# Performance work log

Measured on AMD Instinct MI355X. Metric: run time of the kernel, lower is better.

Reference implementation:

```python
import jax, jax.numpy as jnp
import numpy as np

NSAMPLE = 64
RADIUS = 0.3
HMIN = -0.2
HMAX_LIST = (0.1, 0.2, 0.3, 0.4)
NUM_ANGLE = 12
NUM_DEPTH = 4
EPS = 1e-5


def setup_inputs() -> dict:
    key = jax.random.key(0)
    ks = jax.random.split(key, 32)
    rn = lambda i, s: jax.random.normal(ks[i], s, dtype=jnp.float32)
    ru = lambda i, s: jax.random.uniform(ks[i], s, dtype=jnp.float32)
    return {
        'seed_xyz': rn(0, (2, 1024, 3)),
        'pointcloud': rn(1, (2, 8192, 3)),
        'vp_rot': rn(2, (2, 1024, 3, 3)),
        'cw1': rn(3, (64, 3)), 'cbn1': ru(4, (4, 64)),
        'cw2': rn(5, (128, 64)), 'cbn2': ru(6, (4, 128)),
        'cw3': rn(7, (256, 128)), 'cbn3': ru(8, (4, 256)),
        'ow1': rn(9, (128, 256)), 'ob1': rn(10, (128,)), 'obn1': ru(11, (4, 128)),
        'ow2': rn(12, (128, 128)), 'ob2': rn(13, (128,)), 'obn2': ru(14, (4, 128)),
        'ow3': rn(15, (36, 128)), 'ob3': rn(16, (36,)),
        'tw1': rn(17, (128, 256)), 'tb1': rn(18, (128,)), 'tbn1': ru(19, (4, 128)),
        'tw2': rn(20, (128, 128)), 'tb2': rn(21, (128,)), 'tbn2': ru(22, (4, 128)),
        'tw3': rn(23, (12, 128)), 'tb3': rn(24, (12,)),
    }


def _bn_relu(y, bn):
    g, b, m, v = bn[0], bn[1], bn[2], bn[3]
    return jax.nn.relu(g * (y - m) * jax.lax.rsqrt(v + EPS) + b)


def _bn(y, bn):
    g, b, m, v = bn[0], bn[1], bn[2], bn[3]
    return g * (y - m) * jax.lax.rsqrt(v + EPS) + b


def _forward(seed_xyz, pointcloud, vp_rot, cw1, cbn1, cw2, cbn2, cw3, cbn3,
             ow1, ob1, obn1, ow2, ob2, obn2, ow3, ob3,
             tw1, tb1, tbn1, tw2, tb2, tbn2, tw3, tb3):
    B, ns, _ = seed_xyz.shape
    N = pointcloud.shape[1]
    # relative coords of every scene point w.r.t. every seed, rotated into the
    # grasp-view frame (cylinder axis = x after rotation): (B, ns, N, 3)
    rel = pointcloud[:, None, :, :] - seed_xyz[:, :, None, :]
    rot_rel = jnp.einsum('bsnc,bscd->bsnd', rel, vp_rot)
    ax = rot_rel[..., 0]
    r2 = rot_rel[..., 1] ** 2 + rot_rel[..., 2] ** 2
    pref = jnp.arange(N, dtype=jnp.float32) / N  # earlier index preferred (CUDA scan order)
    groups = []
    for hmax in HMAX_LIST:
        mask = (ax > HMIN) & (ax < hmax) & (r2 < RADIUS * RADIUS)
        score = mask.astype(jnp.float32) * 2.0 - pref
        _, idx = jax.lax.top_k(score, NSAMPLE)  # (B, ns, NSAMPLE), first valid idxs in order
        valid = jnp.take_along_axis(mask, idx, axis=-1)
        idx = jnp.where(valid, idx, idx[..., :1])  # fill slots with first found index
        g = jnp.take_along_axis(rot_rel, idx[..., None], axis=2)  # (B, ns, NSAMPLE, 3)
        groups.append(g)
    feat = jnp.stack(groups, axis=2)  # (B, ns, num_depth, NSAMPLE, 3)
    feat = feat.reshape(B, ns * NUM_DEPTH, NSAMPLE, 3)
    # SharedMLP [3,64,128,256], conv2d 1x1 (no bias) + BN + ReLU
    h = _bn_relu(feat @ cw1.T, cbn1)
    h = _bn_relu(h @ cw2.T, cbn2)
    h = _bn_relu(h @ cw3.T, cbn3)
    vp = jnp.max(h, axis=2)  # max-pool over nsample -> (B, ns*num_depth, 256)

    def head(w1, b1, bn1, w2, b2, bn2, w3, b3):
        x = _bn_relu(vp @ w1.T + b1, bn1)
        x = _bn_relu(x @ w2.T + b2, bn2)
        return x @ w3.T + b3

    op = head(ow1, ob1, obn1, ow2, ob2, obn2, ow3, ob3)     # (B, ns*D, 3*num_angle)
    tol = head(tw1, tb1, tbn1, tw2, tb2, tbn2, tw3, tb3)    # (B, ns*D, num_angle)
    out = jnp.concatenate([op, tol], axis=-1)               # score|angle_cls|width|tolerance
    out = out.reshape(B, ns, NUM_DEPTH, 4 * NUM_ANGLE).transpose(0, 3, 1, 2)
    return out  # (B, 4*num_angle, num_seed, num_depth)


def reference(seed_xyz, pointcloud, vp_rot, cw1, cbn1, cw2, cbn2, cw3, cbn3,
              ow1, ob1, obn1, ow2, ob2, obn2, ow3, ob3,
              tw1, tb1, tbn1, tw2, tb2, tbn2, tw3, tb3):
    return _forward(seed_xyz, pointcloud, vp_rot, cw1, cbn1, cw2, cbn2, cw3, cbn3,
                    ow1, ob1, obn1, ow2, ob2, obn2, ow3, ob3,
                    tw1, tb1, tbn1, tw2, tb2, tbn2, tw3, tb3)
```

## Files before the change

kernel.cpp:

```cpp
#include <hip/hip_runtime.h>
#include <hip/hip_bf16.h>

#define NB    2
#define NS    1024
#define NPTS  8192
#define NGROUP (NB*NS*4)

enum : int {
  OFF_BW2  = 256,
  OFF_W1Q  = 4352,
  OFF_B2   = 8448,
  OFF_BW3  = 8576,
  OFF_B3   = 41344,
  OFF_HB1  = 41600,
  OFF_HB1B = 74368,
  OFF_HB2  = 74624,
  OFF_HB2B = 107392,
  OFF_HB3  = 107648,
  OFF_HB3B = 115840,
  OFF_FEAT = 146688,
  OFF_VP   = 1719552,
  OFF_PCX  = 1719552,
  OFF_PCY  = 1735936,
  OFF_PCZ  = 1752320,
  OFF_SEED = 1768704,
  OFF_ROT  = 1774848,
  OFF_FLAG = 3824896,
  PREP_TOTAL = 189632 + 6144 + 18432 + 49152,
};

struct Ptrs { const void* p[25]; };

typedef __attribute__((ext_vector_type(8))) short bf16x8;
typedef __attribute__((ext_vector_type(4))) float f32x4;
typedef __attribute__((ext_vector_type(4))) unsigned u32x4;

template<typename T> struct LD;
template<> struct LD<float> {
  static __device__ __forceinline__ float get(const void* p, int i){ return ((const float*)p)[i]; }
};
template<> struct LD<__hip_bfloat16> {
  static __device__ __forceinline__ float get(const void* p, int i){ return __bfloat162float(((const __hip_bfloat16*)p)[i]); }
};

template<typename T>
__device__ __forceinline__ float bnscale(const void* bn, int C, int c){
  float g = LD<T>::get(bn, c);
  float v = LD<T>::get(bn, 3*C + c);
  return g / sqrtf(v + 1e-5f);
}

__device__ __forceinline__ unsigned short f2bf(float v){
  __hip_bfloat16 hb = __float2bfloat16(v);
  return *reinterpret_cast<unsigned short*>(&hb);
}

#if __has_builtin(__builtin_amdgcn_cvt_pk_bf16_f32)
typedef __attribute__((ext_vector_type(2))) __bf16 bf16x2_t;
__device__ __forceinline__ unsigned pk2bf(float a, float b){
  bf16x2_t r = __builtin_amdgcn_cvt_pk_bf16_f32(a, b);
  return *reinterpret_cast<unsigned*>(&r);
}
#else
__device__ __forceinline__ unsigned pk2bf(float a, float b){
  return (unsigned)f2bf(a) | ((unsigned)f2bf(b) << 16);
}
#endif

template<typename T>
__device__ void prep_body(const Ptrs& in, float* __restrict__ ws, int i){
  if (i < 256) { int c = i>>2, d = i&3; float s = bnscale<T>(in.p[4],64,c);
    float v = (d<3) ? LD<T>::get(in.p[3], c*3+d)*s
                    : LD<T>::get(in.p[4],64+c) - LD<T>::get(in.p[4],2*64+c)*s;
    ws[OFF_W1Q+i] = v; return; }
  i -= 256;
  if (i < 8192) {
    int j = i&7, f = i>>3, lane = f&63, kn = f>>6, kt = kn&1, nt = kn>>1;
    int n = nt*16 + (lane&15), k = kt*32 + ((lane>>4)<<3) + j;
    float s = bnscale<T>(in.p[6],128,n);
    ((unsigned short*)(ws + OFF_BW2))[i] = f2bf(LD<T>::get(in.p[5], n*64+k)*s); return; }
  i -= 8192;
  if (i < 32768) {
    int j = i&7, f = i>>3, lane = f&63, kn = f>>6, kt = kn&3, nt = kn>>2;
    int n = nt*16 + (lane&15), k = kt*32 + ((lane>>4)<<3) + j;
    float s = bnscale<T>(in.p[8],256,n);
    ((unsigned short*)(ws + OFF_BW3))[i] = f2bf(LD<T>::get(in.p[7], n*128+k)*s); return; }
  i -= 32768;
  if (i < 128) { float s = bnscale<T>(in.p[6],128,i);
    ws[OFF_B2+i] = LD<T>::get(in.p[6],128+i) - LD<T>::get(in.p[6],2*128+i)*s; return; }
  i -= 128;
  if (i < 256) { float s = bnscale<T>(in.p[8],256,i);
    ws[OFF_B3+i] = LD<T>::get(in.p[8],256+i) - LD<T>::get(in.p[8],2*256+i)*s; return; }
  i -= 256;
  if (i < 65536) {
    int j = i&7, f = i>>3, lane = f&63, kn = f>>6, kt = kn&7, nt = kn>>3;
    int n = nt*16 + (lane&15), k = kt*32 + ((lane>>4)<<3) + j;
    float v;
    if (n < 128) v = LD<T>::get(in.p[9],  n*256+k)       * bnscale<T>(in.p[11],128,n);
    else         v = LD<T>::get(in.p[17], (n-128)*256+k) * bnscale<T>(in.p[19],128,n-128);
    ((unsigned short*)(ws + OFF_HB1))[i] = f2bf(v); return; }
  i -= 65536;
  if (i < 256) { int n = i; float v;
    if (n < 128) { float s = bnscale<T>(in.p[11],128,n);
      v = (LD<T>::get(in.p[10],n) - LD<T>::get(in.p[11],2*128+n))*s + LD<T>::get(in.p[11],128+n); }
    else { int m = n-128; float s = bnscale<T>(in.p[19],128,m);
      v = (LD<T>::get(in.p[18],m) - LD<T>::get(in.p[19],2*128+m))*s + LD<T>::get(in.p[19],128+m); }
    ws[OFF_HB1B+n] = v; return; }
  i -= 256;
  if (i < 65536) {
    int j = i&7, f = i>>3, lane = f&63, kn = f>>6, kt = kn&7, nt = kn>>3;
    int n = nt*16 + (lane&15), k = kt*32 + ((lane>>4)<<3) + j;
    float v = 0.f;
    if (n < 128) { if (k < 128)  v = LD<T>::get(in.p[12], n*128+k)            * bnscale<T>(in.p[14],128,n); }
    else         { if (k >= 128) v = LD<T>::get(in.p[20], (n-128)*128+(k-128)) * bnscale<T>(in.p[22],128,n-128); }
    ((unsigned short*)(ws + OFF_HB2))[i] = f2bf(v); return; }
  i -= 65536;
  if (i < 256) { int n = i; float v;
    if (n < 128) { float s = bnscale<T>(in.p[14],128,n);
      v = (LD<T>::get(in.p[13],n) - LD<T>::get(in.p[14],2*128+n))*s + LD<T>::get(in.p[14],128+n); }
    else { int m = n-128; float s = bnscale<T>(in.p[22],128,m);
      v = (LD<T>::get(in.p[21],m) - LD<T>::get(in.p[22],2*128+m))*s + LD<T>::get(in.p[22],128+m); }
    ws[OFF_HB2B+n] = v; return; }
  i -= 256;
  if (i < 16384) {
    int j = i&7, f = i>>3, lane = f&63, kn = f>>6, kt = kn&7, nt = kn>>3;
    int n = nt*16 + (lane&15), k = kt*32 + ((lane>>4)<<3) + j;
    float v = 0.f;
    if (n < 36)      { if (k < 128)  v = LD<T>::get(in.p[15], n*128+k); }
    else if (n < 48) { if (k >= 128) v = LD<T>::get(in.p[23], (n-36)*128+(k-128)); }
    ((unsigned short*)(ws + OFF_HB3))[i] = f2bf(v); return; }
  i -= 16384;
  if (i < 64) { int n = i; float v = 0.f;
    if (n < 36) v = LD<T>::get(in.p[16], n);
    else if (n < 48) v = LD<T>::get(in.p[24], n-36);
    ws[OFF_HB3B+n] = v; return; }
  i -= 64;
  if (i < 6144)  { ws[OFF_SEED+i] = LD<T>::get(in.p[0], i); return; }
  i -= 6144;
  if (i < 18432) { ws[OFF_ROT+i] = LD<T>::get(in.p[2], i); return; }
  i -= 18432;
  {
    int arr = i >> 14, idx = i & 16383;
    ws[OFF_PCX + arr*16384 + idx] = LD<T>::get(in.p[1], idx*3 + arr); }
}

__global__ __launch_bounds__(256) void prep_kernel(Ptrs in, float* __restrict__ ws){
  __shared__ int sf;
  const int t = threadIdx.x;
  if (t == 0) sf = 0;
  __syncthreads();
  int loc = 0;
  const uint4* w3r = (const uint4*)in.p[7];
#pragma unroll
  for (int k = 0; k < 8; ++k) {
    uint4 u = w3r[t + k*256];
    loc |= ((u.x & 0x7F80u) == 0x7F80u) | (((u.x>>16) & 0x7F80u) == 0x7F80u);
    loc |= ((u.y & 0x7F80u) == 0x7F80u) | (((u.y>>16) & 0x7F80u) == 0x7F80u);
    loc |= ((u.z & 0x7F80u) == 0x7F80u) | (((u.z>>16) & 0x7F80u) == 0x7F80u);
    loc |= ((u.w & 0x7F80u) == 0x7F80u) | (((u.w>>16) & 0x7F80u) == 0x7F80u);
  }
  if (loc) atomicOr(&sf, 1);
  __syncthreads();
  const int isf32 = sf;
  const int i = blockIdx.x*256 + t;
  if (i == 0) ((int*)(ws + OFF_FLAG))[0] = isf32;
  if (i >= PREP_TOTAL) return;
  if (isf32) prep_body<float>(in, ws, i);
  else       prep_body<__hip_bfloat16>(in, ws, i);
}

__global__ __launch_bounds__(256) void group_kernel(float* __restrict__ ws){
#pragma clang fp contract(off)
  __shared__ float scratch[2][2][4][192];
  __shared__ int   cl[2][2][4];
  __shared__ float p0s[2][3];
  const int t = threadIdx.x;
  const int wave = t >> 6, lane = t & 63;
  const int s = wave >> 1, half = wave & 1;
  const int seedIdx = blockIdx.x*2 + s;
  const int b = seedIdx >> 10;
  const float sx = ws[OFF_SEED + seedIdx*3+0];
  const float sy = ws[OFF_SEED + seedIdx*3+1];
  const float sz = ws[OFF_SEED + seedIdx*3+2];
  const float r00=ws[OFF_ROT+seedIdx*9+0], r01=ws[OFF_ROT+seedIdx*9+1], r02=ws[OFF_ROT+seedIdx*9+2];
  const float r10=ws[OFF_ROT+seedIdx*9+3], r11=ws[OFF_ROT+seedIdx*9+4], r12=ws[OFF_ROT+seedIdx*9+5];
  const float r20=ws[OFF_ROT+seedIdx*9+6], r21=ws[OFF_ROT+seedIdx*9+7], r22=ws[OFF_ROT+seedIdx*9+8];
  const float* px = ws + OFF_PCX + b*8192;
  const float* py = ws + OFF_PCY + b*8192;
  const float* pz = ws + OFF_PCZ + b*8192;
  if (half == 0 && lane == 0) {
    float e0 = px[0] - sx, e1 = py[0] - sy, e2 = pz[0] - sz;
    p0s[s][0] = e0*r00 + e1*r10 + e2*r20;
    p0s[s][1] = e0*r01 + e1*r11 + e2*r21;
    p0s[s][2] = e0*r02 + e1*r12 + e2*r22;
  }
  float* s0 = scratch[s][half][0];
  float* s1 = scratch[s][half][1];
  float* s2 = scratch[s][half][2];
  float* s3 = scratch[s][half][3];
  int c0n=0, c1n=0, c2n=0, c3n=0;
  const int basept = half*4096;
  const unsigned long long pm = (1ull << lane) - 1ull;

  auto scan = [&](float x, float y, float z){
    float e0 = x - sx, e1 = y - sy, e2 = z - sz;
    float rx = e0*r00 + e1*r10 + e2*r20;
    float ry = e0*r01 + e1*r11 + e2*r21;
    float rz = e0*r02 + e1*r12 + e2*r22;
    float r2 = ry*ry + rz*rz;
    const bool mb = (rx > -0.2f) && (r2 < 0.09f);
    { bool m = mb && (rx < 0.1f); unsigned long long bal = __ballot(m);
      if (bal) { int slot = c0n + __popcll(bal & pm);
        if (m && slot < 64) { s0[slot*3]=rx; s0[slot*3+1]=ry; s0[slot*3+2]=rz; }
        c0n += __popcll(bal); } }
    { bool m = mb && (rx < 0.2f); unsigned long long bal = __ballot(m);
      if (bal) { int slot = c1n + __popcll(bal & pm);
        if (m && slot < 64) { s1[slot*3]=rx; s1[slot*3+1]=ry; s1[slot*3+2]=rz; }
        c1n += __popcll(bal); } }
    { bool m = mb && (rx < 0.3f); unsigned long long bal = __ballot(m);
      if (bal) { int slot = c2n + __popcll(bal & pm);
        if (m && slot < 64) { s2[slot*3]=rx; s2[slot*3+1]=ry; s2[slot*3+2]=rz; }
        c2n += __popcll(bal); } }
    { bool m = mb && (rx < 0.4f); unsigned long long bal = __ballot(m);
      if (bal) { int slot = c3n + __popcll(bal & pm);
        if (m && slot < 64) { s3[slot*3]=rx; s3[slot*3+1]=ry; s3[slot*3+2]=rz; }
        c3n += __popcll(bal); } }
  };

  for (int c = 0; c < 64; c += 2) {
    const int i0 = basept + c*64 + lane;
    float xA = px[i0],    yA = py[i0],    zA = pz[i0];
    float xB = px[i0+64], yB = py[i0+64], zB = pz[i0+64];
    scan(xA, yA, zA);
    scan(xB, yB, zB);
  }
  if (lane == 0) { cl[s][half][0]=c0n; cl[s][half][1]=c1n; cl[s][half][2]=c2n; cl[s][half][3]=c3n; }
  __syncthreads();
  for (int idx = t; idx < 512; idx += 256) {
    const int ss = idx >> 8, bin = (idx >> 6) & 3, slot = idx & 63;
    int ca = cl[ss][0][bin]; if (ca > 64) ca = 64;
    int cb = cl[ss][1][bin];
    const float* A = scratch[ss][0][bin];
    const float* B = scratch[ss][1][bin];
    float fx, fy, fz;
    if (slot < ca)              { fx=A[slot*3]; fy=A[slot*3+1]; fz=A[slot*3+2]; }
    else if (slot - ca < cb)    { int q = slot-ca; fx=B[q*3]; fy=B[q*3+1]; fz=B[q*3+2]; }
    else if (ca > 0)            { fx=A[0]; fy=A[1]; fz=A[2]; }
    else if (cb > 0)            { fx=B[0]; fy=B[1]; fz=B[2]; }
    else                        { fx=p0s[ss][0]; fy=p0s[ss][1]; fz=p0s[ss][2]; }
    const int g = (blockIdx.x*2 + ss)*4 + bin;
    float* fo = ws + OFF_FEAT + g*192;
    fo[slot*3+0]=fx; fo[slot*3+1]=fy; fo[slot*3+2]=fz;
  }
}

__global__ __launch_bounds__(256) void mlp_kernel(float* __restrict__ ws){
  __shared__ unsigned short h2s[2][64*136];
  __shared__ float w1q[4][256];
  const int t = threadIdx.x;
  const int wave = t >> 6, lane = t & 63;
  const int quad = lane >> 4, l15 = lane & 15;
  const int grp = wave >> 1, nhalf = wave & 1;
  const int g = blockIdx.x*2 + grp;
  for (int i = t; i < 1024; i += 256) w1q[i>>8][i&255] = ws[OFF_W1Q + (i&255)];
  const float* feat = ws + OFF_FEAT + g*192;
  __syncthreads();
  float fx[4], fy[4], fz[4];
#pragma unroll
  for (int Nt = 0; Nt < 4; ++Nt) {
    const int sm = Nt*16 + l15;
    fx[Nt] = feat[sm*3+0]; fy[Nt] = feat[sm*3+1]; fz[Nt] = feat[sm*3+2];
  }
  bf16x8 b1[4][2];
  const float* wq = w1q[quad];
#pragma unroll
  for (int kt = 0; kt < 2; ++kt) {
    f32x4 w[8];
#pragma unroll
    for (int j = 0; j < 8; ++j) w[j] = *(const f32x4*)(wq + (kt*32 + quad*8 + j)*4);
#pragma unroll
    for (int Nt = 0; Nt < 4; ++Nt) {
      const float x0 = fx[Nt], x1 = fy[Nt], x2 = fz[Nt];
      u32x4 p;
#pragma unroll
      for (int jp = 0; jp < 4; ++jp) {
        const f32x4 wa = w[2*jp], wb = w[2*jp+1];
        const float v0 = fmaxf(wa[3] + x0*wa[0] + x1*wa[1] + x2*wa[2], 0.f);
        const float v1 = fmaxf(wb[3] + x0*wb[0] + x1*wb[1] + x2*wb[2], 0.f);
        p[jp] = pk2bf(v0, v1);
      }
      b1[Nt][kt] = __builtin_bit_cast(bf16x8, p);
    }
  }
  unsigned short* h2 = h2s[grp];
  const bf16x8* BW2 = (const bf16x8*)(ws + OFF_BW2);
#pragma unroll
  for (int mt4 = 0; mt4 < 4; ++mt4) {
    const int Mt = nhalf*4 + mt4;
    const f32x4 bias4 = *(const f32x4*)(ws + OFF_B2 + Mt*16 + quad*4);
    f32x4 acc[4];
#pragma unroll
    for (int Nt = 0; Nt < 4; ++Nt) acc[Nt] = bias4;
#pragma unroll
    for (int kt = 0; kt < 2; ++kt) {
      const bf16x8 aw = BW2[(Mt*2+kt)*64 + lane];
#pragma unroll
      for (int Nt = 0; Nt < 4; ++Nt)
        acc[Nt] = __builtin_amdgcn_mfma_f32_16x16x32_bf16(aw, b1[Nt][kt], acc[Nt], 0, 0, 0);
    }
#pragma unroll
    for (int Nt = 0; Nt < 4; ++Nt) {
      const unsigned lo = pk2bf(fmaxf(acc[Nt][0],0.f), fmaxf(acc[Nt][1],0.f));
      const unsigned hi = pk2bf(fmaxf(acc[Nt][2],0.f), fmaxf(acc[Nt][3],0.f));
      uint2* dst = (uint2*)&h2[(Nt*16 + l15)*136 + Mt*16 + quad*4];
      *dst = make_uint2(lo, hi);
    }
  }
  __syncthreads();
  bf16x8 a2[4][4];
#pragma unroll
  for (int mt = 0; mt < 4; ++mt)
#pragma unroll
    for (int kt = 0; kt < 4; ++kt)
      a2[mt][kt] = *(const bf16x8*)&h2[(mt*16 + l15)*136 + kt*32 + quad*8];
  const bf16x8* BW3 = (const bf16x8*)(ws + OFF_BW3);
  float vpv[8];
#pragma unroll
  for (int nt8 = 0; nt8 < 8; ++nt8) {
    const int nt = nhalf*8 + nt8;
    const int n = nt*16 + l15;
    const float bias = ws[OFF_B3 + n];
    f32x4 acc[4];
#pragma unroll
    for (int mt = 0; mt < 4; ++mt) acc[mt] = (f32x4){bias, bias, bias, bias};
#pragma unroll
    for (int kt = 0; kt < 4; ++kt) {
      const bf16x8 b = BW3[(nt*4+kt)*64 + lane];
#pragma unroll
      for (int mt = 0; mt < 4; ++mt)
        acc[mt] = __builtin_amdgcn_mfma_f32_16x16x32_bf16(a2[mt][kt], b, acc[mt], 0, 0, 0);
    }
    float mx = 0.f;
#pragma unroll
    for (int mt = 0; mt < 4; ++mt) {
      mx = fmaxf(mx, fmaxf(fmaxf(acc[mt][0], acc[mt][1]), fmaxf(acc[mt][2], acc[mt][3])));
    }
    mx = fmaxf(mx, 0.f);
    mx = fmaxf(mx, __shfl_xor(mx, 16, 64));
    mx = fmaxf(mx, __shfl_xor(mx, 32, 64));
    vpv[nt8] = mx;
  }
  if (quad == 0) {
    float* vp = ws + OFF_VP + g*256 + nhalf*128;
#pragma unroll
    for (int nt8 = 0; nt8 < 8; ++nt8) vp[nt8*16 + l15] = vpv[nt8];
  }
}

#define YSTRIDE 264
__global__ __launch_bounds__(256) void heads_kernel(float* __restrict__ ws, void* __restrict__ outv){
  const int isf32 = ((const volatile int*)(ws + OFF_FLAG))[0];
  __shared__ unsigned short y[16*YSTRIDE];
  const int t = threadIdx.x;
  const int wave = t >> 6, lane = t & 63;
  const int quad = lane >> 4, l15 = lane & 15;
  const int r0 = blockIdx.x * 16;
  bf16x8 a[8];
  const float* vp = ws + OFF_VP + (r0 + l15)*256;
#pragma unroll
  for (int kt = 0; kt < 8; ++kt) {
    const float4* v4 = (const float4*)(vp + kt*32 + quad*8);
    float4 u0 = v4[0], u1 = v4[1];
    a[kt][0]=(short)f2bf(u0.x); a[kt][1]=(short)f2bf(u0.y); a[kt][2]=(short)f2bf(u0.z); a[kt][3]=(short)f2bf(u0.w);
    a[kt][4]=(short)f2bf(u1.x); a[kt][5]=(short)f2bf(u1.y); a[kt][6]=(short)f2bf(u1.z); a[kt][7]=(short)f2bf(u1.w);
  }
  const bf16x8* HB1 = (const bf16x8*)(ws + OFF_HB1);
#pragma unroll
  for (int nt4 = 0; nt4 < 4; ++nt4) {
    const int nt = wave*4 + nt4;
    const int n = nt*16 + l15;
    const float bias = ws[OFF_HB1B + n];
    f32x4 acc = (f32x4){bias, bias, bias, bias};
#pragma unroll
    for (int kt = 0; kt < 8; ++kt)
      acc = __builtin_amdgcn_mfma_f32_16x16x32_bf16(a[kt], HB1[(nt*8+kt)*64 + lane], acc, 0, 0, 0);
#pragma unroll
    for (int jj = 0; jj < 4; ++jj)
      y[(quad*4+jj)*YSTRIDE + n] = f2bf(fmaxf(acc[jj], 0.f));
  }
  __syncthreads();
#pragma unroll
  for (int kt = 0; kt < 8; ++kt)
    a[kt] = *(const bf16x8*)&y[l15*YSTRIDE + kt*32 + quad*8];
  __syncthreads();
  const bf16x8* HB2 = (const bf16x8*)(ws + OFF_HB2);
#pragma unroll
  for (int nt4 = 0; nt4 < 4; ++nt4) {
    const int nt = wave*4 + nt4;
    const int n = nt*16 + l15;
    const float bias = ws[OFF_HB2B + n];
    f32x4 acc = (f32x4){bias, bias, bias, bias};
#pragma unroll
    for (int kt = 0; kt < 8; ++kt)
      acc = __builtin_amdgcn_mfma_f32_16x16x32_bf16(a[kt], HB2[(nt*8+kt)*64 + lane], acc, 0, 0, 0);
#pragma unroll
    for (int jj = 0; jj < 4; ++jj)
      y[(quad*4+jj)*YSTRIDE + n] = f2bf(fmaxf(acc[jj], 0.f));
  }
  __syncthreads();
#pragma unroll
  for (int kt = 0; kt < 8; ++kt)
    a[kt] = *(const bf16x8*)&y[l15*YSTRIDE + kt*32 + quad*8];
  const bf16x8* HB3 = (const bf16x8*)(ws + OFF_HB3);
  {
    const int n = wave*16 + l15;
    const float bias = ws[OFF_HB3B + n];
    f32x4 acc = (f32x4){bias, bias, bias, bias};
#pragma unroll
    for (int kt = 0; kt < 8; ++kt)
      acc = __builtin_amdgcn_mfma_f32_16x16x32_bf16(a[kt], HB3[(wave*8+kt)*64 + lane], acc, 0, 0, 0);
    if (n < 48) {
#pragma unroll
      for (int jj = 0; jj < 4; ++jj) {
        const int gr = r0 + quad*4 + jj;
        const int b = gr >> 12, rem = gr & 4095, s = rem >> 2, d = rem & 3;
        const int o = ((b*48 + n)*1024 + s)*4 + d;
        if (isf32) ((float*)outv)[o] = acc[jj];
        else       ((__hip_bfloat16*)outv)[o] = __float2bfloat16(acc[jj]);
      }
    }
  }
}

extern "C" void kernel_launch(void* const* d_in, const int* in_sizes, int n_in,
                              void* d_out, int out_size, void* d_ws, size_t ws_size,
                              hipStream_t stream) {
  float* ws = (float*)d_ws;
  Ptrs P;
  for (int i = 0; i < 25; ++i) P.p[i] = d_in[i];
  prep_kernel<<<(PREP_TOTAL+255)/256, 256, 0, stream>>>(P, ws);
  group_kernel<<<NB*NS/2, 256, 0, stream>>>(ws);
  mlp_kernel<<<NGROUP/2, 256, 0, stream>>>(ws);
  heads_kernel<<<NGROUP/16, 256, 0, stream>>>(ws, d_out);
}
```

Measured before the change: 204.9 us.

## Bucket groups by valid-sample count and run MLP only on needed row tiles

The grouping kernel now counts valid neighbours per group and atomically appends each group to one of four buckets, keyed by how many 16-row tiles it needs. The MLP kernel is templated on the tile count and launched over all buckets. Each block reads its group ids from the bucket list and only runs the MFMA work for the occupied tiles. This is exact because padded samples repeat an earlier point and cannot change the max-pool. It removes wasted matrix work on sparse groups, at the cost of atomics, an indirect group lookup and many early-exit blocks in an oversized grid.

```diff
diff --git a/kernel.cpp b/kernel.cpp
--- a/kernel.cpp
+++ b/kernel.cpp
@@ -20,12 +20,11 @@
   OFF_HB3B = 115840,
   OFF_FEAT = 146688,
   OFF_VP   = 1719552,
-  OFF_PCX  = 1719552,
-  OFF_PCY  = 1735936,
-  OFF_PCZ  = 1752320,
-  OFF_SEED = 1768704,
-  OFF_ROT  = 1774848,
+  OFF_PCX  = 1719552, OFF_PCY = 1735936, OFF_PCZ = 1752320,
+  OFF_SEED = 1768704, OFF_ROT = 1774848,
   OFF_FLAG = 3824896,
+  OFF_BCNT = 3824900,
+  OFF_BL   = 3824912,
   PREP_TOTAL = 189632 + 6144 + 18432 + 49152,
 };
 
@@ -139,8 +138,7 @@
   i -= 6144;
   if (i < 18432) { ws[OFF_ROT+i] = LD<T>::get(in.p[2], i); return; }
   i -= 18432;
-  {
-    int arr = i >> 14, idx = i & 16383;
+  { int arr = i >> 14, idx = i & 16383;
     ws[OFF_PCX + arr*16384 + idx] = LD<T>::get(in.p[1], idx*3 + arr); }
 }
 
@@ -163,7 +161,10 @@
   __syncthreads();
   const int isf32 = sf;
   const int i = blockIdx.x*256 + t;
-  if (i == 0) ((int*)(ws + OFF_FLAG))[0] = isf32;
+  if (blockIdx.x == 0) {
+    if (t == 0) ((int*)(ws + OFF_FLAG))[0] = isf32;
+    if (t < 4)  ((int*)(ws + OFF_BCNT))[t] = 0;
+  }
   if (i >= PREP_TOTAL) return;
   if (isf32) prep_body<float>(in, ws, i);
   else       prep_body<__hip_bfloat16>(in, ws, i);
@@ -252,34 +253,37 @@
     float* fo = ws + OFF_FEAT + g*192;
     fo[slot*3+0]=fx; fo[slot*3+1]=fy; fo[slot*3+2]=fz;
   }
-}
-
-__global__ __launch_bounds__(256) void mlp_kernel(float* __restrict__ ws){
-  __shared__ unsigned short h2s[2][64*136];
-  __shared__ float w1q[4][256];
-  const int t = threadIdx.x;
-  const int wave = t >> 6, lane = t & 63;
-  const int quad = lane >> 4, l15 = lane & 15;
-  const int grp = wave >> 1, nhalf = wave & 1;
-  const int g = blockIdx.x*2 + grp;
-  for (int i = t; i < 1024; i += 256) w1q[i>>8][i&255] = ws[OFF_W1Q + (i&255)];
+  if (t < 8) {
+    const int ss = t >> 2, bin = t & 3;
+    int tot = cl[ss][0][bin] + cl[ss][1][bin];
+    if (tot > 64) tot = 64;
+    if (tot < 1)  tot = 1;
+    const int mt = (tot + 15) >> 4;
+    const int g = (blockIdx.x*2 + ss)*4 + bin;
+    int w = atomicAdd(&((int*)(ws + OFF_BCNT))[mt-1], 1);
+    if (w < 8192) ((int*)(ws + OFF_BL))[(mt-1)*8192 + w] = g;
+  }
+}
+
+template<int MTS>
+__device__ __forceinline__ void mlp_body(float* __restrict__ ws, unsigned short* __restrict__ h2,
+                                         const float* __restrict__ wq,
+                                         int lane, int quad, int l15, int nhalf, int g){
   const float* feat = ws + OFF_FEAT + g*192;
-  __syncthreads();
-  float fx[4], fy[4], fz[4];
-#pragma unroll
-  for (int Nt = 0; Nt < 4; ++Nt) {
+  float fx[MTS], fy[MTS], fz[MTS];
+#pragma unroll
+  for (int Nt = 0; Nt < MTS; ++Nt) {
     const int sm = Nt*16 + l15;
     fx[Nt] = feat[sm*3+0]; fy[Nt] = feat[sm*3+1]; fz[Nt] = feat[sm*3+2];
   }
-  bf16x8 b1[4][2];
-  const float* wq = w1q[quad];
+  bf16x8 b1[MTS][2];
 #pragma unroll
   for (int kt = 0; kt < 2; ++kt) {
     f32x4 w[8];
 #pragma unroll
     for (int j = 0; j < 8; ++j) w[j] = *(const f32x4*)(wq + (kt*32 + quad*8 + j)*4);
 #pragma unroll
-    for (int Nt = 0; Nt < 4; ++Nt) {
+    for (int Nt = 0; Nt < MTS; ++Nt) {
       const float x0 = fx[Nt], x1 = fy[Nt], x2 = fz[Nt];
       u32x4 p;
 #pragma unroll
@@ -292,24 +296,23 @@
       b1[Nt][kt] = __builtin_bit_cast(bf16x8, p);
     }
   }
-  unsigned short* h2 = h2s[grp];
   const bf16x8* BW2 = (const bf16x8*)(ws + OFF_BW2);
 #pragma unroll
   for (int mt4 = 0; mt4 < 4; ++mt4) {
     const int Mt = nhalf*4 + mt4;
     const f32x4 bias4 = *(const f32x4*)(ws + OFF_B2 + Mt*16 + quad*4);
-    f32x4 acc[4];
-#pragma unroll
-    for (int Nt = 0; Nt < 4; ++Nt) acc[Nt] = bias4;
+    f32x4 acc[MTS];
+#pragma unroll
+    for (int Nt = 0; Nt < MTS; ++Nt) acc[Nt] = bias4;
 #pragma unroll
     for (int kt = 0; kt < 2; ++kt) {
       const bf16x8 aw = BW2[(Mt*2+kt)*64 + lane];
 #pragma unroll
-      for (int Nt = 0; Nt < 4; ++Nt)
+      for (int Nt = 0; Nt < MTS; ++Nt)
         acc[Nt] = __builtin_amdgcn_mfma_f32_16x16x32_bf16(aw, b1[Nt][kt], acc[Nt], 0, 0, 0);
     }
 #pragma unroll
-    for (int Nt = 0; Nt < 4; ++Nt) {
+    for (int Nt = 0; Nt < MTS; ++Nt) {
       const unsigned lo = pk2bf(fmaxf(acc[Nt][0],0.f), fmaxf(acc[Nt][1],0.f));
       const unsigned hi = pk2bf(fmaxf(acc[Nt][2],0.f), fmaxf(acc[Nt][3],0.f));
       uint2* dst = (uint2*)&h2[(Nt*16 + l15)*136 + Mt*16 + quad*4];
@@ -317,9 +320,9 @@
     }
   }
   __syncthreads();
-  bf16x8 a2[4][4];
-#pragma unroll
-  for (int mt = 0; mt < 4; ++mt)
+  bf16x8 a2[MTS][4];
+#pragma unroll
+  for (int mt = 0; mt < MTS; ++mt)
 #pragma unroll
     for (int kt = 0; kt < 4; ++kt)
       a2[mt][kt] = *(const bf16x8*)&h2[(mt*16 + l15)*136 + kt*32 + quad*8];
@@ -330,22 +333,20 @@
     const int nt = nhalf*8 + nt8;
     const int n = nt*16 + l15;
     const float bias = ws[OFF_B3 + n];
-    f32x4 acc[4];
-#pragma unroll
-    for (int mt = 0; mt < 4; ++mt) acc[mt] = (f32x4){bias, bias, bias, bias};
+    f32x4 acc[MTS];
+#pragma unroll
+    for (int mt = 0; mt < MTS; ++mt) acc[mt] = (f32x4){bias, bias, bias, bias};
 #pragma unroll
     for (int kt = 0; kt < 4; ++kt) {
       const bf16x8 b = BW3[(nt*4+kt)*64 + lane];
 #pragma unroll
-      for (int mt = 0; mt < 4; ++mt)
+      for (int mt = 0; mt < MTS; ++mt)
         acc[mt] = __builtin_amdgcn_mfma_f32_16x16x32_bf16(a2[mt][kt], b, acc[mt], 0, 0, 0);
     }
     float mx = 0.f;
 #pragma unroll
-    for (int mt = 0; mt < 4; ++mt) {
+    for (int mt = 0; mt < MTS; ++mt)
       mx = fmaxf(mx, fmaxf(fmaxf(acc[mt][0], acc[mt][1]), fmaxf(acc[mt][2], acc[mt][3])));
-    }
-    mx = fmaxf(mx, 0.f);
     mx = fmaxf(mx, __shfl_xor(mx, 16, 64));
     mx = fmaxf(mx, __shfl_xor(mx, 32, 64));
     vpv[nt8] = mx;
@@ -354,6 +355,35 @@
     float* vp = ws + OFF_VP + g*256 + nhalf*128;
 #pragma unroll
     for (int nt8 = 0; nt8 < 8; ++nt8) vp[nt8*16 + l15] = vpv[nt8];
+  }
+}
+
+__global__ __launch_bounds__(256) void mlp_kernel(float* __restrict__ ws){
+  __shared__ unsigned short h2s[2][64*136];
+  __shared__ float w1q[4][256];
+  const int blk = blockIdx.x;
+  const int v = blk >> 12;
+  const int pairIdx = blk & 4095;
+  int cnt = ((const volatile int*)(ws + OFF_BCNT))[v];
+  if (cnt > 8192) cnt = 8192;
+  if (pairIdx*2 >= cnt) return;
+  const int* lst = (const int*)(ws + OFF_BL) + v*8192;
+  const int g0 = lst[pairIdx*2];
+  const int g1 = (pairIdx*2+1 < cnt) ? lst[pairIdx*2+1] : g0;
+  const int t = threadIdx.x;
+  const int wave = t >> 6, lane = t & 63;
+  const int quad = lane >> 4, l15 = lane & 15;
+  const int grp = wave >> 1, nhalf = wave & 1;
+  const int g = grp ? g1 : g0;
+  for (int i = t; i < 1024; i += 256) w1q[i>>8][i&255] = ws[OFF_W1Q + (i&255)];
+  __syncthreads();
+  unsigned short* h2 = h2s[grp];
+  const float* wq = w1q[quad];
+  switch (v) {
+    case 0: mlp_body<1>(ws, h2, wq, lane, quad, l15, nhalf, g); break;
+    case 1: mlp_body<2>(ws, h2, wq, lane, quad, l15, nhalf, g); break;
+    case 2: mlp_body<3>(ws, h2, wq, lane, quad, l15, nhalf, g); break;
+    default: mlp_body<4>(ws, h2, wq, lane, quad, l15, nhalf, g); break;
   }
 }
 
@@ -440,6 +470,6 @@
   for (int i = 0; i < 25; ++i) P.p[i] = d_in[i];
   prep_kernel<<<(PREP_TOTAL+255)/256, 256, 0, stream>>>(P, ws);
   group_kernel<<<NB*NS/2, 256, 0, stream>>>(ws);
-  mlp_kernel<<<NGROUP/2, 256, 0, stream>>>(ws);
+  mlp_kernel<<<16384, 256, 0, stream>>>(ws);
   heads_kernel<<<NGROUP/16, 256, 0, stream>>>(ws, d_out);
 }
```

Result: slower. 274.1 us (+33.8%).
